# Kernel optimization log

Measured on AMD Instinct MI355X. Metric: run time of the kernel, lower is better.

Reference implementation:

```python
import jax, jax.numpy as jnp
import numpy as np

B, DIM, W0, H0 = 4, 256, 128, 128
HEADS, HEAD_DIM = 8, 32
FOLD, PROP = 2, 4
EPS_GN = 1e-5


def _l2norm(x):
    n = jnp.linalg.norm(x, axis=-1, keepdims=True)
    return x / jnp.maximum(n, 1e-12)  # matches F.normalize eps


def _fold(t, f):
    # (b, c, f*w, f*h) -> (b*f*f, c, w, h), matching einops '(b f1 f2)' ordering
    b, c, W, H = t.shape
    w, h = W // f, H // f
    return t.reshape(b, c, f, w, f, h).transpose(0, 2, 4, 1, 3, 5).reshape(b * f * f, c, w, h)


def _unfold(t, f, b0):
    bf, c, w, h = t.shape
    return t.reshape(b0, f, f, c, w, h).transpose(0, 3, 1, 4, 2, 5).reshape(b0, c, f * w, f * h)


def _pool(t, p):
    # AdaptiveAvgPool2d((p, p)) for divisible sizes
    b, c, w, h = t.shape
    return t.reshape(b, c, p, w // p, p, h // p).mean(axis=(3, 5))


def setup_inputs() -> dict:
    key = jax.random.key(0)
    ks = jax.random.split(key, 6)
    D = HEADS * HEAD_DIM
    return {
        "x": jax.random.normal(ks[0], (B, DIM, W0, H0), jnp.float32),
        "xyz": jax.random.normal(ks[1], (B, 3, W0, H0), jnp.float32),
        "Wv": jax.random.normal(ks[2], (D, DIM, 7, 7), jnp.float32) * 0.02,
        "bv": jnp.zeros((D,), jnp.float32),
        "Wproj": jax.random.normal(ks[3], (DIM, D), jnp.float32) * 0.02,
        "bproj": jnp.zeros((DIM,), jnp.float32),
        "gn_w": jnp.ones((D,), jnp.float32),
        "gn_b": jnp.zeros((D,), jnp.float32),
        "sim_alpha": jnp.ones((1,), jnp.float32),
        "sim_beta": jnp.zeros((1,), jnp.float32),
    }


def reference(x, xyz, Wv, bv, Wproj, bproj, gn_w, gn_b, sim_alpha, sim_beta):
    # value = self.v(x): 7x7 conv, padding 3
    value = jax.lax.conv_general_dilated(
        x, Wv, (1, 1), ((3, 3), (3, 3)),
        dimension_numbers=("NCHW", "OIHW", "NCHW")) + bv[None, :, None, None]
    b0 = x.shape[0]
    # heads split: 'b (e c) w h -> (b e) c w h'
    xh = x.reshape(b0 * HEADS, HEAD_DIM, W0, H0)
    vh = value.reshape(b0 * HEADS, HEAD_DIM, W0, H0)
    xf = _fold(xh, FOLD)
    vf = _fold(vh, FOLD)
    xyzf = _fold(xyz, FOLD)
    bb, c, w, h = xf.shape
    M = PROP * PROP
    N = w * h
    centers = _pool(xf, PROP)                                   # (bb, c, p, p)
    xyz_c = _pool(xyzf, PROP)
    value_centers = _pool(vf, PROP).reshape(bb, c, M).transpose(0, 2, 1)  # (bb, M, c)
    cen = centers.reshape(bb, c, M).transpose(0, 2, 1)          # (bb, M, c)
    xpts = xf.reshape(bb, c, N).transpose(0, 2, 1)              # (bb, N, c)
    vpts = vf.reshape(bb, c, N).transpose(0, 2, 1)              # (bb, N, c)
    sim = jax.nn.sigmoid(sim_beta + sim_alpha *
                         jnp.einsum('bmc,bnc->bmn', _l2norm(cen), _l2norm(xpts)))
    bg = xyzf.shape[0]
    xyz_pts = xyzf.reshape(bg, 3, N).transpose(0, 2, 1)
    xyz_cc = xyz_c.reshape(bg, 3, M).transpose(0, 2, 1)
    sim_geo = jax.nn.sigmoid(sim_beta + sim_alpha *
                             jnp.einsum('bmc,bnc->bmn', _l2norm(xyz_cc), _l2norm(xyz_pts)))
    sim_geo = jnp.tile(sim_geo, (sim.shape[0] // sim_geo.shape[0], 1, 1))  # torch .repeat
    sim = sim * sim_geo ** 2
    # faithful mask math: scatter_(1, argmax, 1.0) into an all-ones tensor leaves it all-ones,
    # so dense_mask == 1 and split_mask == 0 exactly as in the source.
    dense_mask = jnp.ones_like(sim)
    split_mask = 1.0 - dense_mask
    denss_sim = sim * dense_mask
    split_sim = sim * split_mask
    split_out = (jnp.einsum('bmn,bnc->bmc', split_sim, vpts) + value_centers) \
                / (split_sim.sum(-1, keepdims=True) + 1.0)
    denss_out = (jnp.einsum('bmn,bnc->bmc', denss_sim, xpts) + cen) \
                / (denss_sim.sum(-1, keepdims=True) + 1.0)
    denss_pts = jnp.einsum('bmc,bmn->bnc', denss_out, denss_sim)  # (bb, N, c)
    split_pts = jnp.einsum('bmc,bmn->bnc', split_out, split_sim)
    out = (denss_pts + split_pts).transpose(0, 2, 1).reshape(bb, c, w, h)
    out = _unfold(out, FOLD, b0 * HEADS)
    out = out.reshape(b0, HEADS * HEAD_DIM, W0, H0)
    # GroupNorm with 1 group: normalize over (C, H, W) per sample
    mu = out.mean(axis=(1, 2, 3), keepdims=True)
    var = ((out - mu) ** 2).mean(axis=(1, 2, 3), keepdims=True)
    out = (out - mu) / jnp.sqrt(var + EPS_GN)
    out = out * gn_w[None, :, None, None] + gn_b[None, :, None, None]
    # proj 1x1 conv + silu
    out = jnp.einsum('bchw,oc->bohw', out, Wproj) + bproj[None, :, None, None]
    return jax.nn.silu(out)
```

## Files before the change

kernel.cpp:

```cpp
#include <hip/hip_runtime.h>
#include <stdint.h>


typedef __attribute__((ext_vector_type(8))) short short8;
typedef __attribute__((ext_vector_type(4))) float floatx4;
typedef __fp16 fp16x2 __attribute__((ext_vector_type(2)));

#define SIMW 264

__device__ float g_sbp[2048*2];
__device__ float g_alpha[1024];
__device__ float g_bias[1024];
__device__ __attribute__((aligned(16))) _Float16 g_Wa[4*256*256];
__device__ float g_cenraw[128*16*32];
__device__ float g_cenhat[128*16*32];
__device__ float g_gcenhat[16*16*4];
__device__ __attribute__((aligned(16))) _Float16 g_sim[(size_t)128*4096*16];
__device__ float g_dnum[128*16*16*32];
__device__ float g_rsum[128*16*16];
__device__ unsigned g_dnh2[128*256];
__device__ __attribute__((aligned(16))) _Float16 g_preout[(size_t)128*4096*32];

static __device__ __forceinline__ fp16x2 as_h2(unsigned u) { return __builtin_bit_cast(fp16x2, u); }
static __device__ __forceinline__ unsigned pk(float a, float b) {
  return __builtin_bit_cast(unsigned, __builtin_amdgcn_cvt_pkrtz(a, b));
}
#if __has_builtin(__builtin_amdgcn_fdot2)
static __device__ __forceinline__ float fdot2(fp16x2 a, fp16x2 b, float c) {
  return __builtin_amdgcn_fdot2(a, b, c, false);
}
#else
static __device__ __forceinline__ float fdot2(fp16x2 a, fp16x2 b, float c) {
  return c + (float)a[0]*(float)b[0] + (float)a[1]*(float)b[1];
}
#endif
static __device__ __forceinline__ float sum16(const float* p) {
  const float4* q = (const float4*)p;
  float4 a = q[0], b = q[1], c = q[2], d = q[3];
  return (a.x+a.y+a.z+a.w) + (b.x+b.y+b.z+b.w) + (c.x+c.y+c.z+c.w) + (d.x+d.y+d.z+d.w);
}
static __device__ __forceinline__ float sigm(float z) {
  return __builtin_amdgcn_rcpf(1.f + __expf(-z));
}

__global__ __launch_bounds__(64) void k0_geo(const float* __restrict__ xyz) {
  __shared__ float gc[64];
  const int gti = blockIdx.x;
  const int bg = gti >> 2, f1 = (gti >> 1) & 1, f2 = gti & 1;
  const int t = threadIdx.x;
  if (t < 48) {
    const int m = t / 3, ch = t - 3*(t/3);
    const int pi = m >> 2, pj = m & 3;
    const float* p = xyz + (size_t)(bg*3+ch)*16384 + (f1*64 + pi*16)*128 + f2*64 + pj*16;
    float s = 0.f;
    #pragma unroll
    for (int r = 0; r < 16; ++r) s += sum16(p + r*128);
    gc[m*4+ch] = s * (1.f/256.f);
  }
  __syncthreads();
  if (t < 16) {
    float g0 = gc[t*4], g1 = gc[t*4+1], g2 = gc[t*4+2];
    float inv = 1.f / fmaxf(sqrtf(g0*g0+g1*g1+g2*g2), 1e-12f);
    float* o = g_gcenhat + gti*64 + t*4;
    o[0] = g0*inv; o[1] = g1*inv; o[2] = g2*inv; o[3] = 0.f;
  }
}

__global__ __launch_bounds__(128) void k1a_cen(const float* __restrict__ x) {
  __shared__ float cenL[128];
  __shared__ float invL[4];
  const int blk = blockIdx.x;
  const int bb = blk >> 2, pi = blk & 3;
  const int b = bb >> 5, e = (bb >> 2) & 7, f1 = (bb >> 1) & 1, f2 = bb & 1;
  const int tid = threadIdx.x;
  const int c = tid >> 2, pj = tid & 3;
  const int m = pi*4 + pj;
  const float* p = x + ((size_t)(b*256 + e*32 + c)*128 + f1*64 + pi*16)*128 + f2*64 + pj*16;
  float s = 0.f;
  #pragma unroll
  for (int r = 0; r < 16; ++r) s += sum16(p + r*128);
  const float raw = s * (1.f/256.f);
  cenL[pj*32 + c] = raw;
  g_cenraw[(bb*16 + m)*32 + c] = raw;
  __syncthreads();
  if (tid < 4) {
    float ss = 0.f;
    #pragma unroll
    for (int cc = 0; cc < 32; ++cc) { float v = cenL[tid*32+cc]; ss += v*v; }
    invL[tid] = 1.f / fmaxf(sqrtf(ss), 1e-12f);
  }
  __syncthreads();
  g_cenhat[(bb*16 + m)*32 + c] = raw * invL[pj];
}

__global__ __launch_bounds__(256, 4) void k1b_sim(const float* __restrict__ x,
                                                  const float* __restrict__ xyz,
                                                  const float* __restrict__ salpha,
                                                  const float* __restrict__ sbeta) {
  __shared__ __attribute__((aligned(16))) unsigned  xL[256*20];
  __shared__ __attribute__((aligned(16))) _Float16 simS[16*SIMW];
  __shared__ __attribute__((aligned(16))) _Float16 gT[16*SIMW];
  __shared__ __attribute__((aligned(16))) unsigned chP[16*16];
  __shared__ float gcenL[64];
  __shared__ float rsW[4*16];
  __shared__ float dnumL[512];
  const int blk = blockIdx.x;
  const int bb = blk >> 4, ck = blk & 15;
  const int b = bb >> 5, e = (bb >> 2) & 7, f1 = (bb >> 1) & 1, f2 = bb & 1;
  const int gti = ((e & 3) << 2) | (f1 << 1) | f2;
  const int tid = threadIdx.x, lane = tid & 63, wave = tid >> 6;
  const int lm = lane & 15, quad = lane >> 4;
  const float alpha = salpha[0], beta = sbeta[0];
  const float* xt = x + (((size_t)(b*256 + e*32))*128 + f1*64)*128 + f2*64;

  {
    const float2 cp = *(const float2*)(g_cenhat + bb*512 + tid*2);
    chP[tid] = pk(cp.x, cp.y);
  }
  if (tid < 64) gcenL[tid] = g_gcenhat[gti*64 + tid];
  dnumL[tid] = 0.f; dnumL[tid + 256] = 0.f;
  __syncthreads();

  const int ng = ck*256 + tid;
  const int wi = ng >> 6, hi = ng & 63;
  const int addr = wi*128 + hi;
  {
    float ss = 0.f;
    unsigned xp[16];
    #pragma unroll
    for (int p = 0; p < 16; ++p) {
      const float v0 = xt[(size_t)(2*p)*16384 + addr];
      const float v1 = xt[(size_t)(2*p+1)*16384 + addr];
      ss += v0*v0 + v1*v1;
      xp[p] = pk(v0, v1);
    }
    uint4 u0 = {xp[0],xp[1],xp[2],xp[3]};
    uint4 u1 = {xp[4],xp[5],xp[6],xp[7]};
    uint4 u2 = {xp[8],xp[9],xp[10],xp[11]};
    uint4 u3 = {xp[12],xp[13],xp[14],xp[15]};
    *(uint4*)(xL + tid*20)      = u0;
    *(uint4*)(xL + tid*20 + 4)  = u1;
    *(uint4*)(xL + tid*20 + 8)  = u2;
    *(uint4*)(xL + tid*20 + 12) = u3;
    const float invn = __builtin_amdgcn_rcpf(fmaxf(sqrtf(ss), 1e-12f));
    ((float*)xL)[tid*20 + 16] = invn;
  }
  {
    const float* gp = xyz + (size_t)((e & 3)*3)*16384 + (f1*64 + wi)*128 + f2*64 + hi;
    float g0 = gp[0], g1 = gp[16384], g2 = gp[32768];
    const float invg = __builtin_amdgcn_rcpf(fmaxf(sqrtf(g0*g0+g1*g1+g2*g2), 1e-12f));
    g0 *= invg; g1 *= invg; g2 *= invg;
    #pragma unroll
    for (int m = 0; m < 16; ++m) {
      const float* gh = gcenL + m*4;
      const float dg = gh[0]*g0 + gh[1]*g1 + gh[2]*g2;
      const float gg = sigm(beta + alpha*dg);
      gT[m*SIMW + tid] = (_Float16)(gg*gg);
    }
  }
  __syncthreads();

  {
    const short8 afx = *(const short8*)((const _Float16*)chP + lm*32 + quad*8);
    float rsacc[4] = {0.f, 0.f, 0.f, 0.f};
    #pragma unroll
    for (int t = 0; t < 4; ++t) {
      const int px = wave*64 + t*16 + lm;
      const short8 bfx = *(const short8*)((const _Float16*)xL + px*40 + quad*8);
      floatx4 d = {0.f,0.f,0.f,0.f};
      d = __builtin_amdgcn_mfma_f32_16x16x32_f16(afx, bfx, d, 0, 0, 0);
      const float invn = ((const float*)xL)[px*20 + 16];
      #pragma unroll
      for (int r = 0; r < 4; ++r) {
        const int m = quad*4 + r;
        const float gg2 = (float)gT[m*SIMW + px];
        const float sv = sigm(beta + alpha * d[r] * invn) * gg2;
        rsacc[r] += sv;
        simS[m*SIMW + px] = (_Float16)sv;
      }
    }
    #pragma unroll
    for (int r = 0; r < 4; ++r) {
      float v = rsacc[r];
      v += __shfl_xor(v, 1, 64); v += __shfl_xor(v, 2, 64);
      v += __shfl_xor(v, 4, 64); v += __shfl_xor(v, 8, 64);
      if (lm == 0) rsW[wave*16 + quad*4 + r] = v;
    }
  }
  __syncthreads();

  {
    unsigned w[8];
    const unsigned short* sp = (const unsigned short*)simS;
    #pragma unroll
    for (int p = 0; p < 8; ++p)
      w[p] = (unsigned)sp[(2*p)*SIMW + tid] | ((unsigned)sp[(2*p+1)*SIMW + tid] << 16);
    _Float16* gp = g_sim + ((size_t)bb*4096 + ng)*16;
    *(uint4*)gp       = *(const uint4*)&w[0];
    *(uint4*)(gp + 8) = *(const uint4*)&w[4];
  }
  if (tid < 16)
    g_rsum[(bb*16 + ck)*16 + tid] = rsW[tid] + rsW[16+tid] + rsW[32+tid] + rsW[48+tid];

  {
    floatx4 acc0 = {0.f,0.f,0.f,0.f}, acc1 = {0.f,0.f,0.f,0.f};
    #pragma unroll
    for (int ks = 0; ks < 2; ++ks) {
      const int kb = wave*64 + ks*32 + quad*8;
      const short8 af = *(const short8*)(simS + lm*SIMW + kb);
      const int ag = ck*512 + ((kb >> 6)*128) + (kb & 63);
      const float* pb0 = xt + (size_t)lm*16384 + ag;
      const float* pb1 = pb0 + (size_t)16*16384;
      short8 bf0, bf1;
      #pragma unroll
      for (int t = 0; t < 8; ++t) bf0[t] = __builtin_bit_cast(short, (_Float16)pb0[t]);
      #pragma unroll
      for (int t = 0; t < 8; ++t) bf1[t] = __builtin_bit_cast(short, (_Float16)pb1[t]);
      acc0 = __builtin_amdgcn_mfma_f32_16x16x32_f16(af, bf0, acc0, 0, 0, 0);
      acc1 = __builtin_amdgcn_mfma_f32_16x16x32_f16(af, bf1, acc1, 0, 0, 0);
    }
    #pragma unroll
    for (int r = 0; r < 4; ++r) {
      atomicAdd(&dnumL[(quad*4 + r)*32 + lm],      acc0[r]);
      atomicAdd(&dnumL[(quad*4 + r)*32 + 16 + lm], acc1[r]);
    }
  }
  __syncthreads();
  g_dnum[(size_t)(bb*16 + ck)*512 + tid]       = dnumL[tid];
  g_dnum[(size_t)(bb*16 + ck)*512 + 256 + tid] = dnumL[tid + 256];
}

__global__ __launch_bounds__(512) void k1c_red() {
  __shared__ float denssL[512];
  __shared__ float rsL[16];
  const int bb = blockIdx.x, tid = threadIdx.x;
  if (tid < 16) {
    float r = 1.f;
    #pragma unroll
    for (int k = 0; k < 16; ++k) r += g_rsum[(bb*16 + k)*16 + tid];
    rsL[tid] = r;
  }
  float a = g_cenraw[bb*512 + tid];
  #pragma unroll
  for (int k = 0; k < 16; ++k) a += g_dnum[(size_t)bb*8192 + k*512 + tid];
  __syncthreads();
  denssL[tid] = a / rsL[tid >> 5];
  __syncthreads();
  if (tid < 256) {
    const int c = tid >> 3, mp = tid & 7;
    g_dnh2[bb*256 + c*8 + mp] = pk(denssL[(2*mp)*32 + c], denssL[(2*mp+1)*32 + c]);
  }
}

__global__ __launch_bounds__(256, 4) void k1d_out() {
  __shared__ unsigned dl[256];
  __shared__ float sred[8];
  const int blk = blockIdx.x;
  const int bb = blk >> 4, ck = blk & 15;
  const int tid = threadIdx.x, lane = tid & 63, wave = tid >> 6;
  dl[tid] = g_dnh2[bb*256 + tid];
  __syncthreads();
  const int ng = ck*256 + tid;
  unsigned sp[8];
  {
    const _Float16* gp = g_sim + ((size_t)bb*4096 + ng)*16;
    const uint4 q0 = *(const uint4*)gp;
    const uint4 q1 = *(const uint4*)(gp + 8);
    sp[0]=q0.x; sp[1]=q0.y; sp[2]=q0.z; sp[3]=q0.w;
    sp[4]=q1.x; sp[5]=q1.y; sp[6]=q1.z; sp[7]=q1.w;
  }
  float out[32];
  #pragma unroll
  for (int c = 0; c < 32; ++c) {
    float acc = 0.f;
    #pragma unroll
    for (int mp = 0; mp < 8; ++mp) acc = fdot2(as_h2(sp[mp]), as_h2(dl[c*8 + mp]), acc);
    out[c] = acc;
  }
  float s1 = 0.f, s2 = 0.f;
  #pragma unroll
  for (int c = 0; c < 32; ++c) { s1 += out[c]; s2 += out[c]*out[c]; }
  {
    uint4 w[4];
    #pragma unroll
    for (int q = 0; q < 4; ++q) {
      w[q].x = pk(out[8*q+0], out[8*q+1]); w[q].y = pk(out[8*q+2], out[8*q+3]);
      w[q].z = pk(out[8*q+4], out[8*q+5]); w[q].w = pk(out[8*q+6], out[8*q+7]);
    }
    _Float16* gp = g_preout + ((size_t)bb*4096 + ng)*32;
    *(uint4*)gp = w[0]; *(uint4*)(gp+8) = w[1]; *(uint4*)(gp+16) = w[2]; *(uint4*)(gp+24) = w[3];
  }
  #pragma unroll
  for (int off = 1; off < 64; off <<= 1) { s1 += __shfl_xor(s1, off, 64); s2 += __shfl_xor(s2, off, 64); }
  if (lane == 0) { sred[wave] = s1; sred[4+wave] = s2; }
  __syncthreads();
  if (tid == 0) {
    g_sbp[blk*2]   = sred[0]+sred[1]+sred[2]+sred[3];
    g_sbp[blk*2+1] = sred[4]+sred[5]+sred[6]+sred[7];
  }
}

__global__ __launch_bounds__(256) void k2_prep(const float* __restrict__ Wp,
                                               const float* __restrict__ bpr,
                                               const float* __restrict__ gnw,
                                               const float* __restrict__ gnb) {
  __shared__ float betaL[256];
  __shared__ float alphaL[256];
  __shared__ float rr[8];
  const int b = blockIdx.x, t = threadIdx.x, lane = t & 63, wave = t >> 6;
  float s1 = g_sbp[(b*512 + t)*2]     + g_sbp[(b*512 + 256 + t)*2];
  float s2 = g_sbp[(b*512 + t)*2 + 1] + g_sbp[(b*512 + 256 + t)*2 + 1];
  #pragma unroll
  for (int off = 1; off < 64; off <<= 1) { s1 += __shfl_xor(s1, off, 64); s2 += __shfl_xor(s2, off, 64); }
  if (lane == 0) { rr[wave] = s1; rr[4+wave] = s2; }
  __syncthreads();
  const float S1 = rr[0]+rr[1]+rr[2]+rr[3];
  const float S2 = rr[4]+rr[5]+rr[6]+rr[7];
  const float inv_n = 1.f / 4194304.f;
  const float mu  = S1 * inv_n;
  const float inv = rsqrtf(fmaxf(S2*inv_n - mu*mu, 0.f) + 1e-5f);
  const float a = inv * gnw[t];
  g_alpha[b*256 + t] = a;
  alphaL[t] = a;
  betaL[t] = gnb[t] - mu * a;
  __syncthreads();
  float k = bpr[t];
  const float* wr = Wp + t*256;
  _Float16* wa = g_Wa + ((size_t)b*256 + t)*256;
  for (int c = 0; c < 256; c += 8) {
    const float4 w0 = *(const float4*)(wr + c);
    const float4 w1 = *(const float4*)(wr + c + 4);
    k += w0.x*betaL[c+0] + w0.y*betaL[c+1] + w0.z*betaL[c+2] + w0.w*betaL[c+3]
       + w1.x*betaL[c+4] + w1.y*betaL[c+5] + w1.z*betaL[c+6] + w1.w*betaL[c+7];
    uint4 o;
    o.x = pk(w0.x*alphaL[c+0], w0.y*alphaL[c+1]);
    o.y = pk(w0.z*alphaL[c+2], w0.w*alphaL[c+3]);
    o.z = pk(w1.x*alphaL[c+4], w1.y*alphaL[c+5]);
    o.w = pk(w1.z*alphaL[c+6], w1.w*alphaL[c+7]);
    *(uint4*)(wa + c) = o;
  }
  g_bias[b*256 + t] = k;
}

__global__ __launch_bounds__(256, 4) void k3_proj(float* __restrict__ out) {
  __shared__ float biasL[256];
  const int blk = blockIdx.x;
  const int b = blk >> 8, pb = blk & 255;
  const int f1 = pb >> 7, f2 = pb & 1;
  const int nbase = ((pb >> 1) & 63) * 64;
  const int tid = threadIdx.x, lane = tid & 63, wave = tid >> 6;
  const int lm = lane & 15, quad = lane >> 4;
  const int m0 = wave*64;
  biasL[tid] = g_bias[b*256 + tid];
  __syncthreads();
  floatx4 acc[4][4] = {};
  #pragma unroll
  for (int ks = 0; ks < 8; ++ks) {
    const _Float16* bbase = g_preout
        + ((size_t)(b*32 + ks*4 + f1*2 + f2)*4096 + nbase)*32 + quad*8;
    const _Float16* abase = g_Wa + ((size_t)b*256)*256 + (size_t)ks*32 + quad*8;
    short8 afr[4], bfr[4];
    #pragma unroll
    for (int mi = 0; mi < 4; ++mi)
      afr[mi] = *(const short8*)(abase + (size_t)(m0 + mi*16 + lm)*256);
    #pragma unroll
    for (int ni = 0; ni < 4; ++ni)
      bfr[ni] = *(const short8*)(bbase + (ni*16 + lm)*32);
    #pragma unroll
    for (int mi = 0; mi < 4; ++mi) {
      #pragma unroll
      for (int ni = 0; ni < 4; ++ni)
        acc[mi][ni] = __builtin_amdgcn_mfma_f32_16x16x32_f16(afr[mi], bfr[ni], acc[mi][ni], 0, 0, 0);
    }
  }
  #pragma unroll
  for (int mi = 0; mi < 4; ++mi) {
    #pragma unroll
    for (int r = 0; r < 4; ++r) {
      const int o = m0 + mi*16 + quad*4 + r;
      const float kb = biasL[o];
      #pragma unroll
      for (int ni = 0; ni < 4; ++ni) {
        float val = acc[mi][ni][r] + kb;
        val = val * sigm(val);
        out[((size_t)(b*256 + o))*16384 + pb*64 + ni*16 + lm] = val;
      }
    }
  }
}

extern "C" void kernel_launch(void* const* d_in, const int* in_sizes, int n_in,
                              void* d_out, int out_size, void* d_ws, size_t ws_size,
                              hipStream_t stream)
{
  (void)in_sizes; (void)n_in; (void)d_ws; (void)ws_size; (void)out_size;
  const float* x     = (const float*)d_in[0];
  const float* xyz   = (const float*)d_in[1];
  const float* Wproj = (const float*)d_in[4];
  const float* bproj = (const float*)d_in[5];
  const float* gnw   = (const float*)d_in[6];
  const float* gnb   = (const float*)d_in[7];
  const float* sa    = (const float*)d_in[8];
  const float* sb    = (const float*)d_in[9];
  float* out = (float*)d_out;

  hipLaunchKernelGGL(k0_geo,  dim3(16),   dim3(64),  0, stream, xyz);
  hipLaunchKernelGGL(k1a_cen, dim3(512),  dim3(128), 0, stream, x);
  hipLaunchKernelGGL(k1b_sim, dim3(2048), dim3(256), 0, stream, x, xyz, sa, sb);
  hipLaunchKernelGGL(k1c_red, dim3(128),  dim3(512), 0, stream);
  hipLaunchKernelGGL(k1d_out, dim3(2048), dim3(256), 0, stream);
  hipLaunchKernelGGL(k2_prep, dim3(4),    dim3(256), 0, stream, Wproj, bproj, gnw, gnb);
  hipLaunchKernelGGL(k3_proj, dim3(1024), dim3(256), 0, stream, out);
}
```

Baseline: 250.9 us.

## Fuse sim-weighted output into projection kernel and compute GroupNorm stats via Gram matrix

Removes the k1d_out kernel and its fp16 preout buffer in global memory. The per-pixel sim x dense-center product is now computed with MFMA inside the projection kernel and staged in swizzled shared memory. GroupNorm sums are derived analytically: the sum of squares comes from a per-chunk 16x16 Gram matrix of sim (an extra MFMA in k1b) contracted with the dense-center products, and the plain sum comes from row sums. This saves a full write and read of a large intermediate and one launch. In exchange it adds LDS pressure (32KB) in the projection kernel, and the statistics may differ slightly from the fp16-rounded outputs they replace.

```diff
diff --git a/kernel.cpp b/kernel.cpp
--- a/kernel.cpp
+++ b/kernel.cpp
@@ -8,8 +8,7 @@
 
 #define SIMW 264
 
-__device__ float g_sbp[2048*2];
-__device__ float g_alpha[1024];
+__device__ float g_sbp[256];
 __device__ float g_bias[1024];
 __device__ __attribute__((aligned(16))) _Float16 g_Wa[4*256*256];
 __device__ float g_cenraw[128*16*32];
@@ -17,13 +16,16 @@
 __device__ float g_gcenhat[16*16*4];
 __device__ __attribute__((aligned(16))) _Float16 g_sim[(size_t)128*4096*16];
 __device__ float g_dnum[128*16*16*32];
+__device__ float g_Gp[(size_t)128*16*256];
 __device__ float g_rsum[128*16*16];
-__device__ unsigned g_dnh2[128*256];
-__device__ __attribute__((aligned(16))) _Float16 g_preout[(size_t)128*4096*32];
+__device__ __attribute__((aligned(16))) unsigned g_dnh2[128*256];
 
 static __device__ __forceinline__ fp16x2 as_h2(unsigned u) { return __builtin_bit_cast(fp16x2, u); }
 static __device__ __forceinline__ unsigned pk(float a, float b) {
   return __builtin_bit_cast(unsigned, __builtin_amdgcn_cvt_pkrtz(a, b));
+}
+static __device__ __forceinline__ float h16(float v) {
+  return (float)as_h2(pk(v, 0.f))[0];
 }
 #if __has_builtin(__builtin_amdgcn_fdot2)
 static __device__ __forceinline__ float fdot2(fp16x2 a, fp16x2 b, float c) {
@@ -104,6 +106,7 @@
   __shared__ float gcenL[64];
   __shared__ float rsW[4*16];
   __shared__ float dnumL[512];
+  float* GL = (float*)gT;
   const int blk = blockIdx.x;
   const int bb = blk >> 4, ck = blk & 15;
   const int b = bb >> 5, e = (bb >> 2) & 7, f1 = (bb >> 1) & 1, f2 = bb & 1;
@@ -188,6 +191,8 @@
     }
   }
   __syncthreads();
+  if (tid < 256) GL[tid] = 0.f;
+  __syncthreads();
 
   {
     unsigned w[8];
@@ -204,6 +209,7 @@
 
   {
     floatx4 acc0 = {0.f,0.f,0.f,0.f}, acc1 = {0.f,0.f,0.f,0.f};
+    floatx4 accG = {0.f,0.f,0.f,0.f};
     #pragma unroll
     for (int ks = 0; ks < 2; ++ks) {
       const int kb = wave*64 + ks*32 + quad*8;
@@ -218,22 +224,26 @@
       for (int t = 0; t < 8; ++t) bf1[t] = __builtin_bit_cast(short, (_Float16)pb1[t]);
       acc0 = __builtin_amdgcn_mfma_f32_16x16x32_f16(af, bf0, acc0, 0, 0, 0);
       acc1 = __builtin_amdgcn_mfma_f32_16x16x32_f16(af, bf1, acc1, 0, 0, 0);
+      accG = __builtin_amdgcn_mfma_f32_16x16x32_f16(af, af,  accG, 0, 0, 0);
     }
     #pragma unroll
     for (int r = 0; r < 4; ++r) {
       atomicAdd(&dnumL[(quad*4 + r)*32 + lm],      acc0[r]);
       atomicAdd(&dnumL[(quad*4 + r)*32 + 16 + lm], acc1[r]);
+      atomicAdd(&GL[(quad*4 + r)*16 + lm],         accG[r]);
     }
   }
   __syncthreads();
   g_dnum[(size_t)(bb*16 + ck)*512 + tid]       = dnumL[tid];
   g_dnum[(size_t)(bb*16 + ck)*512 + 256 + tid] = dnumL[tid + 256];
+  g_Gp[(size_t)(bb*16 + ck)*256 + tid]         = GL[tid];
 }
 
 __global__ __launch_bounds__(512) void k1c_red() {
   __shared__ float denssL[512];
   __shared__ float rsL[16];
-  const int bb = blockIdx.x, tid = threadIdx.x;
+  __shared__ float red[16];
+  const int bb = blockIdx.x, tid = threadIdx.x, lane = tid & 63, wv = tid >> 6;
   if (tid < 16) {
     float r = 1.f;
     #pragma unroll
@@ -250,53 +260,38 @@
     const int c = tid >> 3, mp = tid & 7;
     g_dnh2[bb*256 + c*8 + mp] = pk(denssL[(2*mp)*32 + c], denssL[(2*mp+1)*32 + c]);
   }
-}
-
-__global__ __launch_bounds__(256, 4) void k1d_out() {
-  __shared__ unsigned dl[256];
-  __shared__ float sred[8];
-  const int blk = blockIdx.x;
-  const int bb = blk >> 4, ck = blk & 15;
-  const int tid = threadIdx.x, lane = tid & 63, wave = tid >> 6;
-  dl[tid] = g_dnh2[bb*256 + tid];
-  __syncthreads();
-  const int ng = ck*256 + tid;
-  unsigned sp[8];
-  {
-    const _Float16* gp = g_sim + ((size_t)bb*4096 + ng)*16;
-    const uint4 q0 = *(const uint4*)gp;
-    const uint4 q1 = *(const uint4*)(gp + 8);
-    sp[0]=q0.x; sp[1]=q0.y; sp[2]=q0.z; sp[3]=q0.w;
-    sp[4]=q1.x; sp[5]=q1.y; sp[6]=q1.z; sp[7]=q1.w;
-  }
-  float out[32];
-  #pragma unroll
-  for (int c = 0; c < 32; ++c) {
-    float acc = 0.f;
-    #pragma unroll
-    for (int mp = 0; mp < 8; ++mp) acc = fdot2(as_h2(sp[mp]), as_h2(dl[c*8 + mp]), acc);
-    out[c] = acc;
-  }
-  float s1 = 0.f, s2 = 0.f;
-  #pragma unroll
-  for (int c = 0; c < 32; ++c) { s1 += out[c]; s2 += out[c]*out[c]; }
-  {
-    uint4 w[4];
-    #pragma unroll
-    for (int q = 0; q < 4; ++q) {
-      w[q].x = pk(out[8*q+0], out[8*q+1]); w[q].y = pk(out[8*q+2], out[8*q+3]);
-      w[q].z = pk(out[8*q+4], out[8*q+5]); w[q].w = pk(out[8*q+6], out[8*q+7]);
-    }
-    _Float16* gp = g_preout + ((size_t)bb*4096 + ng)*32;
-    *(uint4*)gp = w[0]; *(uint4*)(gp+8) = w[1]; *(uint4*)(gp+16) = w[2]; *(uint4*)(gp+24) = w[3];
-  }
-  #pragma unroll
-  for (int off = 1; off < 64; off <<= 1) { s1 += __shfl_xor(s1, off, 64); s2 += __shfl_xor(s2, off, 64); }
-  if (lane == 0) { sred[wave] = s1; sred[4+wave] = s2; }
+  float contrib = 0.f;
+  if (tid < 256) {
+    const int m = tid >> 4, m2 = tid & 15;
+    float g = 0.f;
+    #pragma unroll
+    for (int k = 0; k < 16; ++k) g += g_Gp[((size_t)bb*16 + k)*256 + tid];
+    float p = 0.f;
+    #pragma unroll
+    for (int c = 0; c < 32; ++c)
+      p += h16(denssL[m*32 + c]) * h16(denssL[m2*32 + c]);
+    contrib = g * p;
+  }
+  float s1t = 0.f;
+  if (tid < 16) {
+    float sc = 0.f;
+    #pragma unroll
+    for (int c = 0; c < 32; ++c) sc += h16(denssL[tid*32 + c]);
+    s1t = (rsL[tid] - 1.f) * sc;
+  }
+  #pragma unroll
+  for (int off = 1; off < 64; off <<= 1) {
+    contrib += __shfl_xor(contrib, off, 64);
+    s1t     += __shfl_xor(s1t, off, 64);
+  }
+  if (lane == 0) { red[wv] = contrib; red[8 + wv] = s1t; }
   __syncthreads();
   if (tid == 0) {
-    g_sbp[blk*2]   = sred[0]+sred[1]+sred[2]+sred[3];
-    g_sbp[blk*2+1] = sred[4]+sred[5]+sred[6]+sred[7];
+    float s2 = 0.f, s1 = 0.f;
+    #pragma unroll
+    for (int w = 0; w < 8; ++w) { s2 += red[w]; s1 += red[8 + w]; }
+    g_sbp[bb*2]     = s1;
+    g_sbp[bb*2 + 1] = s2;
   }
 }
 
@@ -306,21 +301,22 @@
                                                const float* __restrict__ gnb) {
   __shared__ float betaL[256];
   __shared__ float alphaL[256];
-  __shared__ float rr[8];
-  const int b = blockIdx.x, t = threadIdx.x, lane = t & 63, wave = t >> 6;
-  float s1 = g_sbp[(b*512 + t)*2]     + g_sbp[(b*512 + 256 + t)*2];
-  float s2 = g_sbp[(b*512 + t)*2 + 1] + g_sbp[(b*512 + 256 + t)*2 + 1];
-  #pragma unroll
-  for (int off = 1; off < 64; off <<= 1) { s1 += __shfl_xor(s1, off, 64); s2 += __shfl_xor(s2, off, 64); }
-  if (lane == 0) { rr[wave] = s1; rr[4+wave] = s2; }
-  __syncthreads();
-  const float S1 = rr[0]+rr[1]+rr[2]+rr[3];
-  const float S2 = rr[4]+rr[5]+rr[6]+rr[7];
+  __shared__ float S12[2];
+  const int b = blockIdx.x, t = threadIdx.x;
+  if (t < 64) {
+    float v1 = 0.f, v2 = 0.f;
+    if (t < 32) { v1 = g_sbp[(b*32 + t)*2]; v2 = g_sbp[(b*32 + t)*2 + 1]; }
+    #pragma unroll
+    for (int off = 1; off < 64; off <<= 1) { v1 += __shfl_xor(v1, off, 64); v2 += __shfl_xor(v2, off, 64); }
+    if (t == 0) { S12[0] = v1; S12[1] = v2; }
+  }
+  __syncthreads();
+  const float S1 = S12[0];
+  const float S2 = S12[1];
   const float inv_n = 1.f / 4194304.f;
   const float mu  = S1 * inv_n;
   const float inv = rsqrtf(fmaxf(S2*inv_n - mu*mu, 0.f) + 1e-5f);
   const float a = inv * gnw[t];
-  g_alpha[b*256 + t] = a;
   alphaL[t] = a;
   betaL[t] = gnb[t] - mu * a;
   __syncthreads();
@@ -342,7 +338,8 @@
   g_bias[b*256 + t] = k;
 }
 
-__global__ __launch_bounds__(256, 4) void k3_proj(float* __restrict__ out) {
+__global__ __launch_bounds__(256, 4) void kf_proj(float* __restrict__ out) {
+  __shared__ __attribute__((aligned(16))) _Float16 preL[64*256];
   __shared__ float biasL[256];
   const int blk = blockIdx.x;
   const int b = blk >> 8, pb = blk & 255;
@@ -352,20 +349,51 @@
   const int lm = lane & 15, quad = lane >> 4;
   const int m0 = wave*64;
   biasL[tid] = g_bias[b*256 + tid];
-  __syncthreads();
+
+  #pragma unroll
+  for (int eh = 0; eh < 2; ++eh) {
+    const int e = wave*2 + eh;
+    const int bb = b*32 + e*4 + f1*2 + f2;
+    short8 bf0 = {}, bf1 = {};
+    if (quad < 2) {
+      const _Float16* dp = (const _Float16*)g_dnh2 + (size_t)bb*512 + quad*8;
+      bf0 = *(const short8*)(dp + lm*16);
+      bf1 = *(const short8*)(dp + (16 + lm)*16);
+    }
+    #pragma unroll
+    for (int pt = 0; pt < 4; ++pt) {
+      const short8 af = *(const short8*)(g_sim
+          + ((size_t)bb*4096 + nbase + pt*16 + lm)*16 + (quad & 1)*8);
+      floatx4 c0 = {0.f,0.f,0.f,0.f}, c1 = {0.f,0.f,0.f,0.f};
+      c0 = __builtin_amdgcn_mfma_f32_16x16x32_f16(af, bf0, c0, 0, 0, 0);
+      c1 = __builtin_amdgcn_mfma_f32_16x16x32_f16(af, bf1, c1, 0, 0, 0);
+      #pragma unroll
+      for (int r = 0; r < 4; ++r) {
+        const int px = pt*16 + quad*4 + r;
+        const int swz = (px & 7) << 4;
+        const int b0 = (px*512 + (e*32 + lm)*2) ^ swz;
+        const int b1 = (px*512 + (e*32 + 16 + lm)*2) ^ swz;
+        *(_Float16*)((char*)preL + b0) = (_Float16)c0[r];
+        *(_Float16*)((char*)preL + b1) = (_Float16)c1[r];
+      }
+    }
+  }
+  __syncthreads();
+
   floatx4 acc[4][4] = {};
   #pragma unroll
   for (int ks = 0; ks < 8; ++ks) {
-    const _Float16* bbase = g_preout
-        + ((size_t)(b*32 + ks*4 + f1*2 + f2)*4096 + nbase)*32 + quad*8;
     const _Float16* abase = g_Wa + ((size_t)b*256)*256 + (size_t)ks*32 + quad*8;
     short8 afr[4], bfr[4];
     #pragma unroll
     for (int mi = 0; mi < 4; ++mi)
       afr[mi] = *(const short8*)(abase + (size_t)(m0 + mi*16 + lm)*256);
     #pragma unroll
-    for (int ni = 0; ni < 4; ++ni)
-      bfr[ni] = *(const short8*)(bbase + (ni*16 + lm)*32);
+    for (int ni = 0; ni < 4; ++ni) {
+      const int row = ni*16 + lm;
+      const int byte = (row*512 + ks*64 + quad*16) ^ ((row & 7) << 4);
+      bfr[ni] = *(const short8*)((const char*)preL + byte);
+    }
     #pragma unroll
     for (int mi = 0; mi < 4; ++mi) {
       #pragma unroll
@@ -408,7 +436,6 @@
   hipLaunchKernelGGL(k1a_cen, dim3(512),  dim3(128), 0, stream, x);
   hipLaunchKernelGGL(k1b_sim, dim3(2048), dim3(256), 0, stream, x, xyz, sa, sb);
   hipLaunchKernelGGL(k1c_red, dim3(128),  dim3(512), 0, stream);
-  hipLaunchKernelGGL(k1d_out, dim3(2048), dim3(256), 0, stream);
   hipLaunchKernelGGL(k2_prep, dim3(4),    dim3(256), 0, stream, Wproj, bproj, gnw, gnb);
-  hipLaunchKernelGGL(k3_proj, dim3(1024), dim3(256), 0, stream, out);
-}
+  hipLaunchKernelGGL(kf_proj, dim3(1024), dim3(256), 0, stream, out);
+}
```

Result: slower. 260.1 us (+3.7%).
